# Optimization experiments

Hardware: AMD Instinct MI355X
Metric: run time of the kernel (lower is better)

The kernel has to match this reference:

```python
import jax, jax.numpy as jnp
import numpy as np

C = 64
K = 3  # kernel_size
B, H, W = 8, 128, 128


def conv2d(x, w, b, pad, groups=1):
    y = jax.lax.conv_general_dilated(
        x, w, window_strides=(1, 1), padding=[(pad, pad), (pad, pad)],
        feature_group_count=groups, dimension_numbers=('NCHW', 'OIHW', 'NCHW'))
    return y + b[None, :, None, None]


def setup_inputs() -> dict:
    key = jax.random.key(0)
    ks = jax.random.split(key, 11)
    s3 = 1.0 / np.sqrt(C * 9)  # kaiming-ish scale for 3x3 convs
    inp = {
        'x':  jax.random.normal(ks[0], (B, C, H, W), jnp.float32),
        'w0': jax.random.normal(ks[1], (C, C, 3, 3), jnp.float32) * s3,
        'b0': jax.random.normal(ks[2], (C,), jnp.float32) * 0.01,
        'w1': jax.random.normal(ks[3], (C, 1, 3, 3), jnp.float32) * (1.0 / 3.0),  # depthwise
        'b1': jax.random.normal(ks[4], (C,), jnp.float32) * 0.01,
        'w2': jax.random.normal(ks[5], (1, 1, K), jnp.float32) * (1.0 / np.sqrt(K)),  # conv1d over channel axis
        'b2': jax.random.normal(ks[6], (1,), jnp.float32) * 0.01,
        'w3': jax.random.normal(ks[7], (C * K * K, C, 1, 1), jnp.float32) * (1.0 / np.sqrt(C)),  # 1x1 -> dynamic filters
        'b3': jax.random.normal(ks[8], (C * K * K,), jnp.float32) * 0.01,
        'wf': jax.random.normal(ks[9], (C, C, 3, 3), jnp.float32) * s3,
        'bf': jax.random.normal(ks[10], (C,), jnp.float32) * 0.01,
    }
    return inp


def reference(x, w0, b0, w1, b1, w2, b2, w3, b3, wf, bf):
    b, c, h, w = x.shape
    pre = x
    # conv0: dense 3x3
    x0 = conv2d(x, w0, b0, pad=1)
    # conv1: depthwise 3x3
    x1 = conv2d(x0, w1, b1, pad=1, groups=c)
    # ECA-style channel attention: global avg pool -> conv1d over channel dim
    m = jnp.mean(x0, axis=(2, 3))  # [b, c]
    x2 = jax.lax.conv_general_dilated(
        m[:, None, :], w2, window_strides=(1,), padding=[(K // 2, K // 2)],
        dimension_numbers=('NCH', 'OIH', 'NCH')) + b2[None, :, None]  # [b, 1, c]
    out = x1 + x2[:, 0, :, None, None]  # broadcast [b,c,1,1] over h,w
    # conv3: 1x1 producing per-pixel dynamic filters [b, c*9, h, w]
    fil = jnp.einsum('oc,bchw->bohw', w3[:, :, 0, 0], out) + b3[None, :, None, None]
    filter_x = fil.reshape(b, c, K * K, h, w)
    # unfold(x0): 3x3 patches, channel-major then row-major kernel positions
    xp = jnp.pad(x0, ((0, 0), (0, 0), (1, 1), (1, 1)))
    unfold_x = jnp.stack(
        [xp[:, :, i:i + h, j:j + w] for i in range(3) for j in range(3)], axis=2)  # [b,c,9,h,w]
    out = jnp.sum(unfold_x * filter_x, axis=2)  # per-pixel dynamic conv
    out = jnp.where(out >= 0, out, 0.2 * out)  # LeakyReLU(0.2)
    out = conv2d(out, wf, bf, pad=1) + pre
    return out
```

## Files before the change

kernel.cpp:

```cpp
#include <hip/hip_runtime.h>

#define BB 8
#define C 64
#define HH 128
#define WW 128
#define HW (HH*WW)

#define TS 72
#define NPX 324

typedef __attribute__((ext_vector_type(8))) short short8;
typedef __attribute__((ext_vector_type(4))) float f32x4;

__device__ inline unsigned short f2bf(float f) {
    union { float f; unsigned u; } v; v.f = f;
    unsigned r = v.u + 0x7fff + ((v.u >> 16) & 1);
    return (unsigned short)(r >> 16);
}
__device__ inline float bf2f(unsigned short h) {
    union { unsigned u; float f; } v; v.u = ((unsigned)h) << 16;
    return v.f;
}

__global__ __launch_bounds__(256) void prep_kernel(
    const float* __restrict__ w0, const float* __restrict__ wf,
    const float* __restrict__ w3, const float* __restrict__ b3,
    unsigned short* __restrict__ wb0, unsigned short* __restrict__ wbf,
    unsigned short* __restrict__ wb3, float* __restrict__ b3r,
    float* __restrict__ m)
{
    const int t = blockIdx.x * 256 + threadIdx.x;
    for (int i = t; i < C*C*9; i += 32*256) {
        int p = i % 9; int rest = i / 9; int ci = rest % C; int oc = rest / C;
        wb0[(p*C + oc)*C + ci] = f2bf(w0[i]);
        wbf[(p*C + oc)*C + ci] = f2bf(wf[i]);
    }
    for (int i = t; i < 9*C*C; i += 32*256) {
        int j = i >> 12, oc = (i >> 6) & 63, k = i & 63;
        wb3[i] = f2bf(w3[(oc*9 + j)*C + k]);
    }
    for (int i = t; i < 9*C; i += 32*256) {
        int j = i >> 6, oc = i & 63;
        b3r[i] = b3[oc*9 + j];
    }
    for (int i = t; i < BB*C; i += 32*256) m[i] = 0.f;
}

template<bool FIRST>
__global__ __launch_bounds__(256) void conv_mfma_kernel(
    const void* __restrict__ in,
    const unsigned short* __restrict__ wb,
    const float* __restrict__ bias,
    const float* __restrict__ res,
    void* __restrict__ outp)
{
    __shared__ unsigned short tile[NPX*TS];
    const int b  = blockIdx.z;
    const int h0 = blockIdx.y * 16;
    const int w0 = blockIdx.x * 16;
    const int t  = threadIdx.x;

    {
        const int pxi = t & 31, g = t >> 5;
        for (int px = pxi; px < NPX; px += 32) {
            int th = px / 18, tw = px - th*18;
            int gh = h0 + th - 1, gw = w0 + tw - 1;
            short8 v = {0,0,0,0,0,0,0,0};
            if ((unsigned)gh < HH && (unsigned)gw < WW) {
                if (FIRST) {
                    const float* sp = (const float*)in
                        + ((size_t)(b*C + g*8)*HW + gh*WW + gw);
#pragma unroll
                    for (int k = 0; k < 8; ++k) v[k] = (short)f2bf(sp[k*HW]);
                } else {
                    v = *(const short8*)((const unsigned short*)in
                        + ((size_t)(b*HW) + gh*WW + gw)*C + g*8);
                }
            }
            *(short8*)&tile[px*TS + g*8] = v;
        }
    }
    __syncthreads();

    const int wid = t >> 6, ln = t & 63;
    const int l15 = ln & 15, q = ln >> 4;

    f32x4 acc[4][4];
#pragma unroll
    for (int mg = 0; mg < 4; ++mg)
#pragma unroll
        for (int nt = 0; nt < 4; ++nt) acc[mg][nt] = (f32x4){0.f,0.f,0.f,0.f};

#pragma unroll
    for (int p = 0; p < 9; ++p) {
        const int dh = p / 3, dw = p % 3;
#pragma unroll
        for (int ks = 0; ks < 2; ++ks) {
            short8 bfrag[4];
#pragma unroll
            for (int nt = 0; nt < 4; ++nt)
                bfrag[nt] = *(const short8*)&wb[((size_t)(p*C) + nt*16 + l15)*C + ks*32 + q*8];
            short8 afrag[4];
#pragma unroll
            for (int mg = 0; mg < 4; ++mg) {
                const int r = wid*4 + mg;
                afrag[mg] = *(const short8*)&tile[((r+dh)*18 + l15 + dw)*TS + ks*32 + q*8];
            }
#pragma unroll
            for (int mg = 0; mg < 4; ++mg)
#pragma unroll
                for (int nt = 0; nt < 4; ++nt)
                    acc[mg][nt] = __builtin_amdgcn_mfma_f32_16x16x32_bf16(
                        afrag[mg], bfrag[nt], acc[mg][nt], 0, 0, 0);
        }
    }

    if (FIRST) {
        unsigned short* x0 = (unsigned short*)outp;
#pragma unroll
        for (int mg = 0; mg < 4; ++mg) {
            const int hh = h0 + wid*4 + mg;
#pragma unroll
            for (int nt = 0; nt < 4; ++nt) {
                const int oc = nt*16 + l15;
                const float bv = bias[oc];
#pragma unroll
                for (int reg = 0; reg < 4; ++reg) {
                    const int wwp = w0 + q*4 + reg;
                    x0[((size_t)(b*HW) + hh*WW + wwp)*C + oc] = f2bf(acc[mg][nt][reg] + bv);
                }
            }
        }
    } else {
        float* outg = (float*)outp;
#pragma unroll
        for (int mg = 0; mg < 4; ++mg) {
            const int hh = h0 + wid*4 + mg;
#pragma unroll
            for (int nt = 0; nt < 4; ++nt) {
                const int oc = nt*16 + l15;
                const float bv = bias[oc];
                const size_t base = (size_t)(b*C + oc)*HW + hh*WW + w0 + q*4;
                const float4 rv = *(const float4*)&res[base];
                float4 ov;
                ov.x = acc[mg][nt][0] + bv + rv.x;
                ov.y = acc[mg][nt][1] + bv + rv.y;
                ov.z = acc[mg][nt][2] + bv + rv.z;
                ov.w = acc[mg][nt][3] + bv + rv.w;
                *(float4*)&outg[base] = ov;
            }
        }
    }
}

__global__ __launch_bounds__(256) void mean_kernel(
    const unsigned short* __restrict__ x0, float* __restrict__ m)
{
    const int b = blockIdx.x >> 4, slice = blockIdx.x & 15;
    const int t = threadIdx.x;
    const int pxi = t >> 3, g = t & 7;
    const unsigned short* base = x0 + ((size_t)b*HW + slice*1024)*C + g*8;
    float s[8];
#pragma unroll
    for (int k = 0; k < 8; ++k) s[k] = 0.f;
    for (int it = 0; it < 32; ++it) {
        short8 v = *(const short8*)&base[(size_t)(it*32 + pxi)*C];
#pragma unroll
        for (int k = 0; k < 8; ++k) s[k] += bf2f((unsigned short)v[k]);
    }
    __shared__ float red[32][64];
#pragma unroll
    for (int k = 0; k < 8; ++k) red[pxi][g*8+k] = s[k];
    __syncthreads();
    if (t < 64) {
        float acc = 0.f;
        for (int i = 0; i < 32; ++i) acc += red[i][t];
        atomicAdd(&m[b*C + t], acc * (1.f/(float)HW));
    }
}

__global__ __launch_bounds__(256) void fused_kernel(
    const unsigned short* __restrict__ x0,
    const float* __restrict__ w1, const float* __restrict__ b1,
    const float* __restrict__ w2, const float* __restrict__ b2,
    const unsigned short* __restrict__ wb3,
    const float* __restrict__ b3r,
    const float* __restrict__ m,
    unsigned short* __restrict__ y)
{
    __shared__ unsigned short tile[NPX*TS];
    __shared__ unsigned short alds[256*64];
    const int b  = blockIdx.z;
    const int h0 = blockIdx.y * 16;
    const int w0 = blockIdx.x * 16;
    const int t  = threadIdx.x;

    {
        const int pxi = t & 31, g = t >> 5;
        for (int px = pxi; px < NPX; px += 32) {
            int th = px / 18, tw = px - th*18;
            int gh = h0 + th - 1, gw = w0 + tw - 1;
            short8 v = {0,0,0,0,0,0,0,0};
            if ((unsigned)gh < HH && (unsigned)gw < WW)
                v = *(const short8*)&x0[((size_t)(b*HW) + gh*WW + gw)*C + g*8];
            *(short8*)&tile[px*TS + g*8] = v;
        }
    }
    __syncthreads();

    const int r = t >> 4, cc = t & 15;
    const unsigned short* tbase = tile + (r*18 + cc)*TS;

    float outv[64];
    const float w2a = w2[0], w2b = w2[1], w2c = w2[2], b2v = b2[0];
#pragma unroll
    for (int g = 0; g < 8; ++g) {
        float dw8[8];
#pragma unroll
        for (int k = 0; k < 8; ++k) dw8[k] = 0.f;
#pragma unroll
        for (int j = 0; j < 9; ++j) {
            short8 v = *(const short8*)&tbase[((j/3)*18 + (j%3))*TS + g*8];
#pragma unroll
            for (int k = 0; k < 8; ++k)
                dw8[k] = fmaf(w1[(g*8+k)*9 + j], bf2f((unsigned short)v[k]), dw8[k]);
        }
#pragma unroll
        for (int k = 0; k < 8; ++k) {
            const int c = g*8 + k;
            const float mc = m[b*C + c];
            const float mp = (c > 0)  ? m[b*C + c - 1] : 0.f;
            const float mn = (c < 63) ? m[b*C + c + 1] : 0.f;
            outv[c] = dw8[k] + b1[c] + fmaf(w2a, mp, fmaf(w2b, mc, fmaf(w2c, mn, b2v)));
        }
    }

    {
        const int sw = t & 7;
#pragma unroll
        for (int g = 0; g < 8; ++g) {
            short8 v;
#pragma unroll
            for (int k = 0; k < 8; ++k) v[k] = (short)f2bf(outv[g*8 + k]);
            *(short8*)&alds[t*64 + ((g ^ sw) * 8)] = v;
        }
    }
    __syncthreads();

    const int wid = t >> 6, ln = t & 63;
    const int l15 = ln & 15, q = ln >> 4;

    short8 afrag[4][2];
#pragma unroll
    for (int mg = 0; mg < 4; ++mg) {
        const int px = (wid*4 + mg)*16 + l15;
        const int sw = px & 7;
#pragma unroll
        for (int ks = 0; ks < 2; ++ks)
            afrag[mg][ks] = *(const short8*)&alds[px*64 + (((ks*4 + q) ^ sw) * 8)];
    }

    f32x4 y_acc[4][4];
#pragma unroll
    for (int mg = 0; mg < 4; ++mg)
#pragma unroll
        for (int nt = 0; nt < 4; ++nt) y_acc[mg][nt] = (f32x4){0.f,0.f,0.f,0.f};

#pragma unroll
    for (int j = 0; j < 9; ++j) {
        const int dh = j / 3, dw = j % 3;
#pragma unroll
        for (int ntoc = 0; ntoc < 4; ++ntoc) {
            const int oc = ntoc*16 + l15;
            const float b3v = b3r[j*64 + oc];
            const short8 bf0 = *(const short8*)&wb3[((size_t)(j*64 + oc))*64 + q*8];
            const short8 bf1 = *(const short8*)&wb3[((size_t)(j*64 + oc))*64 + 32 + q*8];
            f32x4 fil[4];
#pragma unroll
            for (int mg = 0; mg < 4; ++mg) {
                f32x4 a = (f32x4){b3v, b3v, b3v, b3v};
                a = __builtin_amdgcn_mfma_f32_16x16x32_bf16(afrag[mg][0], bf0, a, 0, 0, 0);
                a = __builtin_amdgcn_mfma_f32_16x16x32_bf16(afrag[mg][1], bf1, a, 0, 0, 0);
                fil[mg] = a;
            }
#pragma unroll
            for (int mg = 0; mg < 4; ++mg) {
                const int rr = wid*4 + mg;
                const unsigned short* pb = &tile[((rr+dh)*18 + q*4 + dw)*TS + oc];
#pragma unroll
                for (int reg = 0; reg < 4; ++reg) {
                    const float pv = bf2f(pb[reg*TS]);
                    y_acc[mg][ntoc][reg] = fmaf(fil[mg][reg], pv, y_acc[mg][ntoc][reg]);
                }
            }
        }
    }

    __syncthreads();
    unsigned short* ybuf = alds;
#pragma unroll
    for (int mg = 0; mg < 4; ++mg) {
        const int rr = wid*4 + mg;
#pragma unroll
        for (int ntoc = 0; ntoc < 4; ++ntoc) {
            const int oc = ntoc*16 + l15;
#pragma unroll
            for (int reg = 0; reg < 4; ++reg) {
                float v = y_acc[mg][ntoc][reg];
                v = (v >= 0.f) ? v : 0.2f * v;
                ybuf[(rr*16 + q*4 + reg)*64 + oc] = f2bf(v);
            }
        }
    }
    __syncthreads();
    for (int id = t; id < 2048; id += 256) {
        int px = id >> 3, g = id & 7;
        short8 v = *(const short8*)&ybuf[px*64 + g*8];
        int rr = px >> 4, cw = px & 15;
        *(short8*)&y[((size_t)(b*HW) + (h0+rr)*WW + (w0+cw))*C + g*8] = v;
    }
}

extern "C" void kernel_launch(void* const* d_in, const int* in_sizes, int n_in,
                              void* d_out, int out_size, void* d_ws, size_t ws_size,
                              hipStream_t stream) {
    const float* x  = (const float*)d_in[0];
    const float* w0 = (const float*)d_in[1];
    const float* b0 = (const float*)d_in[2];
    const float* w1 = (const float*)d_in[3];
    const float* b1 = (const float*)d_in[4];
    const float* w2 = (const float*)d_in[5];
    const float* b2 = (const float*)d_in[6];
    const float* w3 = (const float*)d_in[7];
    const float* b3 = (const float*)d_in[8];
    const float* wf = (const float*)d_in[9];
    const float* bf = (const float*)d_in[10];
    float* out = (float*)d_out;

    unsigned short* x0  = (unsigned short*)d_ws;
    unsigned short* y   = x0 + (size_t)BB*HW*C;
    float*          m   = (float*)(y + (size_t)BB*HW*C);
    unsigned short* wb0 = (unsigned short*)(m + BB*C);
    unsigned short* wbf = wb0 + 9*C*C;
    unsigned short* wb3 = wbf + 9*C*C;
    float*          b3r = (float*)(wb3 + 9*C*C);

    prep_kernel<<<32, 256, 0, stream>>>(w0, wf, w3, b3, wb0, wbf, wb3, b3r, m);
    conv_mfma_kernel<true><<<dim3(8,8,8), 256, 0, stream>>>(x, wb0, b0, nullptr, x0);
    mean_kernel<<<128, 256, 0, stream>>>(x0, m);
    fused_kernel<<<dim3(8,8,8), 256, 0, stream>>>(x0, w1, b1, w2, b2, wb3, b3r, m, y);
    conv_mfma_kernel<false><<<dim3(8,8,8), 256, 0, stream>>>(y, wbf, bf, x, out);
}
```

Baseline: 223.7 us.

## Fuse channel mean into conv0 epilogue and double threads per block

The channel mean is now computed in the first conv's epilogue with shuffle reductions and atomics, so the separate mean kernel and its re-read of x0 are gone. All three main kernels go from 256 to 512 threads per block, splitting output channels (conv) or rows (fused) across more waves. The fused kernel precomputes the attention bias once per block, uses a transposed depthwise-weight layout for vector loads, swaps MFMA operands so pixel values load as vectors, and swizzles the y staging buffer. In exchange, each wave gets less work, and each conv block now issues 64 extra atomics.

```diff
diff --git a/kernel.cpp b/kernel.cpp
--- a/kernel.cpp
+++ b/kernel.cpp
@@ -10,6 +10,7 @@
 #define NPX 324
 
 typedef __attribute__((ext_vector_type(8))) short short8;
+typedef __attribute__((ext_vector_type(4))) unsigned short us4;
 typedef __attribute__((ext_vector_type(4))) float f32x4;
 
 __device__ inline unsigned short f2bf(float f) {
@@ -25,9 +26,10 @@
 __global__ __launch_bounds__(256) void prep_kernel(
     const float* __restrict__ w0, const float* __restrict__ wf,
     const float* __restrict__ w3, const float* __restrict__ b3,
+    const float* __restrict__ w1,
     unsigned short* __restrict__ wb0, unsigned short* __restrict__ wbf,
     unsigned short* __restrict__ wb3, float* __restrict__ b3r,
-    float* __restrict__ m)
+    float* __restrict__ w1r, float* __restrict__ m)
 {
     const int t = blockIdx.x * 256 + threadIdx.x;
     for (int i = t; i < C*C*9; i += 32*256) {
@@ -40,29 +42,32 @@
         wb3[i] = f2bf(w3[(oc*9 + j)*C + k]);
     }
     for (int i = t; i < 9*C; i += 32*256) {
-        int j = i >> 6, oc = i & 63;
-        b3r[i] = b3[oc*9 + j];
+        int j = i >> 6, c = i & 63;
+        b3r[i] = b3[c*9 + j];
+        w1r[i] = w1[c*9 + j];
     }
     for (int i = t; i < BB*C; i += 32*256) m[i] = 0.f;
 }
 
 template<bool FIRST>
-__global__ __launch_bounds__(256) void conv_mfma_kernel(
+__global__ __launch_bounds__(512, 4) void conv_mfma_kernel(
     const void* __restrict__ in,
     const unsigned short* __restrict__ wb,
     const float* __restrict__ bias,
     const float* __restrict__ res,
-    void* __restrict__ outp)
+    void* __restrict__ outp,
+    float* __restrict__ m)
 {
-    __shared__ unsigned short tile[NPX*TS];
+    __shared__ __align__(16) unsigned short tile[NPX*TS];
+    __shared__ __align__(16) float sred[2][2][4][16];
     const int b  = blockIdx.z;
     const int h0 = blockIdx.y * 16;
     const int w0 = blockIdx.x * 16;
     const int t  = threadIdx.x;
 
     {
-        const int pxi = t & 31, g = t >> 5;
-        for (int px = pxi; px < NPX; px += 32) {
+        const int pxi = t & 63, g = t >> 6;
+        for (int px = pxi; px < NPX; px += 64) {
             int th = px / 18, tw = px - th*18;
             int gh = h0 + th - 1, gw = w0 + tw - 1;
             short8 v = {0,0,0,0,0,0,0,0};
@@ -84,61 +89,73 @@
 
     const int wid = t >> 6, ln = t & 63;
     const int l15 = ln & 15, q = ln >> 4;
-
-    f32x4 acc[4][4];
+    const int ng = wid & 1, wr = wid >> 1;
+
+    f32x4 acc[4][2];
 #pragma unroll
     for (int mg = 0; mg < 4; ++mg)
 #pragma unroll
-        for (int nt = 0; nt < 4; ++nt) acc[mg][nt] = (f32x4){0.f,0.f,0.f,0.f};
+        for (int nt = 0; nt < 2; ++nt) acc[mg][nt] = (f32x4){0.f,0.f,0.f,0.f};
 
 #pragma unroll
     for (int p = 0; p < 9; ++p) {
         const int dh = p / 3, dw = p % 3;
 #pragma unroll
         for (int ks = 0; ks < 2; ++ks) {
-            short8 bfrag[4];
-#pragma unroll
-            for (int nt = 0; nt < 4; ++nt)
-                bfrag[nt] = *(const short8*)&wb[((size_t)(p*C) + nt*16 + l15)*C + ks*32 + q*8];
+            short8 bfrag[2];
+#pragma unroll
+            for (int nt = 0; nt < 2; ++nt)
+                bfrag[nt] = *(const short8*)&wb[((size_t)(p*C) + ng*32 + nt*16 + l15)*C + ks*32 + q*8];
             short8 afrag[4];
 #pragma unroll
-            for (int mg = 0; mg < 4; ++mg) {
-                const int r = wid*4 + mg;
-                afrag[mg] = *(const short8*)&tile[((r+dh)*18 + l15 + dw)*TS + ks*32 + q*8];
-            }
-#pragma unroll
             for (int mg = 0; mg < 4; ++mg)
-#pragma unroll
-                for (int nt = 0; nt < 4; ++nt)
+                afrag[mg] = *(const short8*)&tile[((wr*4 + mg + dh)*18 + l15 + dw)*TS + ks*32 + q*8];
+#pragma unroll
+            for (int mg = 0; mg < 4; ++mg)
+#pragma unroll
+                for (int nt = 0; nt < 2; ++nt)
                     acc[mg][nt] = __builtin_amdgcn_mfma_f32_16x16x32_bf16(
                         afrag[mg], bfrag[nt], acc[mg][nt], 0, 0, 0);
         }
     }
 
     if (FIRST) {
-        unsigned short* x0 = (unsigned short*)outp;
-#pragma unroll
-        for (int mg = 0; mg < 4; ++mg) {
-            const int hh = h0 + wid*4 + mg;
-#pragma unroll
-            for (int nt = 0; nt < 4; ++nt) {
-                const int oc = nt*16 + l15;
-                const float bv = bias[oc];
+        unsigned short* x0o = (unsigned short*)outp;
+#pragma unroll
+        for (int nt = 0; nt < 2; ++nt) {
+            const int oc = ng*32 + nt*16 + l15;
+            const float bv = bias[oc];
+            float s = 0.f;
+#pragma unroll
+            for (int mg = 0; mg < 4; ++mg) {
+                const int hh = h0 + wr*4 + mg;
 #pragma unroll
                 for (int reg = 0; reg < 4; ++reg) {
                     const int wwp = w0 + q*4 + reg;
-                    x0[((size_t)(b*HW) + hh*WW + wwp)*C + oc] = f2bf(acc[mg][nt][reg] + bv);
+                    const unsigned short sv = f2bf(acc[mg][nt][reg] + bv);
+                    x0o[((size_t)(b*HW) + hh*WW + wwp)*C + oc] = sv;
+                    s += bf2f(sv);
                 }
             }
+            s += __shfl_xor(s, 16);
+            s += __shfl_xor(s, 32);
+            if (q == 0) sred[ng][nt][wr][l15] = s;
+        }
+        __syncthreads();
+        if (t < 64) {
+            const int g2 = t >> 5, nt2 = (t >> 4) & 1, l2 = t & 15;
+            float s = sred[g2][nt2][0][l2] + sred[g2][nt2][1][l2]
+                    + sred[g2][nt2][2][l2] + sred[g2][nt2][3][l2];
+            atomicAdd(&m[b*C + t], s * (1.f/(float)HW));
         }
     } else {
         float* outg = (float*)outp;
 #pragma unroll
         for (int mg = 0; mg < 4; ++mg) {
-            const int hh = h0 + wid*4 + mg;
-#pragma unroll
-            for (int nt = 0; nt < 4; ++nt) {
-                const int oc = nt*16 + l15;
+            const int hh = h0 + wr*4 + mg;
+#pragma unroll
+            for (int nt = 0; nt < 2; ++nt) {
+                const int oc = ng*32 + nt*16 + l15;
                 const float bv = bias[oc];
                 const size_t base = (size_t)(b*C + oc)*HW + hh*WW + w0 + q*4;
                 const float4 rv = *(const float4*)&res[base];
@@ -153,51 +170,33 @@
     }
 }
 
-__global__ __launch_bounds__(256) void mean_kernel(
-    const unsigned short* __restrict__ x0, float* __restrict__ m)
-{
-    const int b = blockIdx.x >> 4, slice = blockIdx.x & 15;
-    const int t = threadIdx.x;
-    const int pxi = t >> 3, g = t & 7;
-    const unsigned short* base = x0 + ((size_t)b*HW + slice*1024)*C + g*8;
-    float s[8];
-#pragma unroll
-    for (int k = 0; k < 8; ++k) s[k] = 0.f;
-    for (int it = 0; it < 32; ++it) {
-        short8 v = *(const short8*)&base[(size_t)(it*32 + pxi)*C];
-#pragma unroll
-        for (int k = 0; k < 8; ++k) s[k] += bf2f((unsigned short)v[k]);
-    }
-    __shared__ float red[32][64];
-#pragma unroll
-    for (int k = 0; k < 8; ++k) red[pxi][g*8+k] = s[k];
-    __syncthreads();
-    if (t < 64) {
-        float acc = 0.f;
-        for (int i = 0; i < 32; ++i) acc += red[i][t];
-        atomicAdd(&m[b*C + t], acc * (1.f/(float)HW));
-    }
-}
-
-__global__ __launch_bounds__(256) void fused_kernel(
+__global__ __launch_bounds__(512, 4) void fused_kernel(
     const unsigned short* __restrict__ x0,
-    const float* __restrict__ w1, const float* __restrict__ b1,
+    const float* __restrict__ w1r,
+    const float* __restrict__ b1,
     const float* __restrict__ w2, const float* __restrict__ b2,
     const unsigned short* __restrict__ wb3,
     const float* __restrict__ b3r,
     const float* __restrict__ m,
     unsigned short* __restrict__ y)
 {
-    __shared__ unsigned short tile[NPX*TS];
-    __shared__ unsigned short alds[256*64];
+    __shared__ __align__(16) unsigned short tile[NPX*TS];
+    __shared__ __align__(16) unsigned short alds[256*64];
+    __shared__ __align__(16) float att[64];
     const int b  = blockIdx.z;
     const int h0 = blockIdx.y * 16;
     const int w0 = blockIdx.x * 16;
     const int t  = threadIdx.x;
 
+    if (t < 64) {
+        const float mc = m[b*C + t];
+        const float mp = (t > 0)  ? m[b*C + t - 1] : 0.f;
+        const float mn = (t < 63) ? m[b*C + t + 1] : 0.f;
+        att[t] = b1[t] + fmaf(w2[0], mp, fmaf(w2[1], mc, fmaf(w2[2], mn, b2[0])));
+    }
     {
-        const int pxi = t & 31, g = t >> 5;
-        for (int px = pxi; px < NPX; px += 32) {
+        const int pxi = t & 63, g = t >> 6;
+        for (int px = pxi; px < NPX; px += 64) {
             int th = px / 18, tw = px - th*18;
             int gh = h0 + th - 1, gw = w0 + tw - 1;
             short8 v = {0,0,0,0,0,0,0,0};
@@ -208,41 +207,33 @@
     }
     __syncthreads();
 
-    const int r = t >> 4, cc = t & 15;
-    const unsigned short* tbase = tile + (r*18 + cc)*TS;
-
-    float outv[64];
-    const float w2a = w2[0], w2b = w2[1], w2c = w2[2], b2v = b2[0];
-#pragma unroll
-    for (int g = 0; g < 8; ++g) {
-        float dw8[8];
-#pragma unroll
-        for (int k = 0; k < 8; ++k) dw8[k] = 0.f;
-#pragma unroll
-        for (int j = 0; j < 9; ++j) {
-            short8 v = *(const short8*)&tbase[((j/3)*18 + (j%3))*TS + g*8];
-#pragma unroll
-            for (int k = 0; k < 8; ++k)
-                dw8[k] = fmaf(w1[(g*8+k)*9 + j], bf2f((unsigned short)v[k]), dw8[k]);
-        }
-#pragma unroll
-        for (int k = 0; k < 8; ++k) {
-            const int c = g*8 + k;
-            const float mc = m[b*C + c];
-            const float mp = (c > 0)  ? m[b*C + c - 1] : 0.f;
-            const float mn = (c < 63) ? m[b*C + c + 1] : 0.f;
-            outv[c] = dw8[k] + b1[c] + fmaf(w2a, mp, fmaf(w2b, mc, fmaf(w2c, mn, b2v)));
-        }
-    }
-
     {
-        const int sw = t & 7;
-#pragma unroll
-        for (int g = 0; g < 8; ++g) {
-            short8 v;
-#pragma unroll
-            for (int k = 0; k < 8; ++k) v[k] = (short)f2bf(outv[g*8 + k]);
-            *(short8*)&alds[t*64 + ((g ^ sw) * 8)] = v;
+        const int px1 = t >> 1, chalf = t & 1;
+        const int r1 = px1 >> 4, c1 = px1 & 15;
+        const unsigned short* tbase = tile + (r1*18 + c1)*TS + chalf*32;
+        const int sw1 = px1 & 7;
+#pragma unroll
+        for (int g = 0; g < 4; ++g) {
+            const f32x4 a0 = *(const f32x4*)&att[chalf*32 + g*8];
+            const f32x4 a1 = *(const f32x4*)&att[chalf*32 + g*8 + 4];
+            float dw8[8];
+#pragma unroll
+            for (int k = 0; k < 8; ++k) dw8[k] = (k < 4) ? a0[k] : a1[k-4];
+#pragma unroll
+            for (int j = 0; j < 9; ++j) {
+                short8 v = *(const short8*)&tbase[((j/3)*18 + (j%3))*TS + g*8];
+                const f32x4 wv0 = *(const f32x4*)&w1r[j*64 + chalf*32 + g*8];
+                const f32x4 wv1 = *(const f32x4*)&w1r[j*64 + chalf*32 + g*8 + 4];
+#pragma unroll
+                for (int k = 0; k < 8; ++k)
+                    dw8[k] = fmaf((k < 4) ? wv0[k] : wv1[k-4],
+                                  bf2f((unsigned short)v[k]), dw8[k]);
+            }
+            short8 ov;
+#pragma unroll
+            for (int k = 0; k < 8; ++k) ov[k] = (short)f2bf(dw8[k]);
+            const int kg = chalf*4 + g;
+            *(short8*)&alds[px1*64 + ((kg ^ sw1) * 8)] = ov;
         }
     }
     __syncthreads();
@@ -250,19 +241,19 @@
     const int wid = t >> 6, ln = t & 63;
     const int l15 = ln & 15, q = ln >> 4;
 
-    short8 afrag[4][2];
-#pragma unroll
-    for (int mg = 0; mg < 4; ++mg) {
-        const int px = (wid*4 + mg)*16 + l15;
+    short8 afrag[2][2];
+#pragma unroll
+    for (int mg = 0; mg < 2; ++mg) {
+        const int px = (wid*2 + mg)*16 + l15;
         const int sw = px & 7;
 #pragma unroll
         for (int ks = 0; ks < 2; ++ks)
             afrag[mg][ks] = *(const short8*)&alds[px*64 + (((ks*4 + q) ^ sw) * 8)];
     }
 
-    f32x4 y_acc[4][4];
-#pragma unroll
-    for (int mg = 0; mg < 4; ++mg)
+    f32x4 y_acc[2][4];
+#pragma unroll
+    for (int mg = 0; mg < 2; ++mg)
 #pragma unroll
         for (int nt = 0; nt < 4; ++nt) y_acc[mg][nt] = (f32x4){0.f,0.f,0.f,0.f};
 
@@ -271,27 +262,20 @@
         const int dh = j / 3, dw = j % 3;
 #pragma unroll
         for (int ntoc = 0; ntoc < 4; ++ntoc) {
-            const int oc = ntoc*16 + l15;
-            const float b3v = b3r[j*64 + oc];
-            const short8 bf0 = *(const short8*)&wb3[((size_t)(j*64 + oc))*64 + q*8];
-            const short8 bf1 = *(const short8*)&wb3[((size_t)(j*64 + oc))*64 + 32 + q*8];
-            f32x4 fil[4];
-#pragma unroll
-            for (int mg = 0; mg < 4; ++mg) {
-                f32x4 a = (f32x4){b3v, b3v, b3v, b3v};
-                a = __builtin_amdgcn_mfma_f32_16x16x32_bf16(afrag[mg][0], bf0, a, 0, 0, 0);
-                a = __builtin_amdgcn_mfma_f32_16x16x32_bf16(afrag[mg][1], bf1, a, 0, 0, 0);
-                fil[mg] = a;
-            }
-#pragma unroll
-            for (int mg = 0; mg < 4; ++mg) {
-                const int rr = wid*4 + mg;
-                const unsigned short* pb = &tile[((rr+dh)*18 + q*4 + dw)*TS + oc];
-#pragma unroll
-                for (int reg = 0; reg < 4; ++reg) {
-                    const float pv = bf2f(pb[reg*TS]);
-                    y_acc[mg][ntoc][reg] = fmaf(fil[mg][reg], pv, y_acc[mg][ntoc][reg]);
-                }
+            const short8 bf0 = *(const short8*)&wb3[((size_t)(j*64 + ntoc*16 + l15))*64 + q*8];
+            const short8 bf1 = *(const short8*)&wb3[((size_t)(j*64 + ntoc*16 + l15))*64 + 32 + q*8];
+            const f32x4 b3v4 = *(const f32x4*)&b3r[j*64 + ntoc*16 + q*4];
+#pragma unroll
+            for (int mg = 0; mg < 2; ++mg) {
+                f32x4 a = b3v4;
+                a = __builtin_amdgcn_mfma_f32_16x16x32_bf16(bf0, afrag[mg][0], a, 0, 0, 0);
+                a = __builtin_amdgcn_mfma_f32_16x16x32_bf16(bf1, afrag[mg][1], a, 0, 0, 0);
+                const int rr = wid*2 + mg;
+                const us4 pv = *(const us4*)
+                    &tile[((rr+dh)*18 + l15 + dw)*TS + ntoc*16 + q*4];
+#pragma unroll
+                for (int reg = 0; reg < 4; ++reg)
+                    y_acc[mg][ntoc][reg] = fmaf(a[reg], bf2f(pv[reg]), y_acc[mg][ntoc][reg]);
             }
         }
     }
@@ -299,23 +283,28 @@
     __syncthreads();
     unsigned short* ybuf = alds;
 #pragma unroll
-    for (int mg = 0; mg < 4; ++mg) {
-        const int rr = wid*4 + mg;
+    for (int mg = 0; mg < 2; ++mg) {
+        const int rr = wid*2 + mg;
+        const int px = rr*16 + l15;
+        const int swy = (px & 7) << 1;
 #pragma unroll
         for (int ntoc = 0; ntoc < 4; ++ntoc) {
-            const int oc = ntoc*16 + l15;
+            us4 ov;
 #pragma unroll
             for (int reg = 0; reg < 4; ++reg) {
                 float v = y_acc[mg][ntoc][reg];
                 v = (v >= 0.f) ? v : 0.2f * v;
-                ybuf[(rr*16 + q*4 + reg)*64 + oc] = f2bf(v);
-            }
-        }
-    }
-    __syncthreads();
-    for (int id = t; id < 2048; id += 256) {
+                ov[reg] = f2bf(v);
+            }
+            const int slot = (ntoc*4 + q) ^ swy;
+            *(us4*)&ybuf[px*64 + slot*4] = ov;
+        }
+    }
+    __syncthreads();
+    for (int id = t; id < 2048; id += 512) {
         int px = id >> 3, g = id & 7;
-        short8 v = *(const short8*)&ybuf[px*64 + g*8];
+        const int swy = (px & 7) << 1;
+        short8 v = *(const short8*)&ybuf[px*64 + ((2*g) ^ swy)*4];
         int rr = px >> 4, cw = px & 15;
         *(short8*)&y[((size_t)(b*HW) + (h0+rr)*WW + (w0+cw))*C + g*8] = v;
     }
@@ -344,10 +333,10 @@
     unsigned short* wbf = wb0 + 9*C*C;
     unsigned short* wb3 = wbf + 9*C*C;
     float*          b3r = (float*)(wb3 + 9*C*C);
-
-    prep_kernel<<<32, 256, 0, stream>>>(w0, wf, w3, b3, wb0, wbf, wb3, b3r, m);
-    conv_mfma_kernel<true><<<dim3(8,8,8), 256, 0, stream>>>(x, wb0, b0, nullptr, x0);
-    mean_kernel<<<128, 256, 0, stream>>>(x0, m);
-    fused_kernel<<<dim3(8,8,8), 256, 0, stream>>>(x0, w1, b1, w2, b2, wb3, b3r, m, y);
-    conv_mfma_kernel<false><<<dim3(8,8,8), 256, 0, stream>>>(y, wbf, bf, x, out);
-}
+    float*          w1r = b3r + 9*C;
+
+    prep_kernel<<<32, 256, 0, stream>>>(w0, wf, w3, b3, w1, wb0, wbf, wb3, b3r, w1r, m);
+    conv_mfma_kernel<true><<<dim3(8,8,8), 512, 0, stream>>>(x, wb0, b0, nullptr, x0, m);
+    fused_kernel<<<dim3(8,8,8), 512, 0, stream>>>(x0, w1r, b1, w2, b2, wb3, b3r, m, y);
+    conv_mfma_kernel<false><<<dim3(8,8,8), 512, 0, stream>>>(y, wbf, bf, x, out, nullptr);
+}
```

Result: slower. 352.7 us (+57.7%).

## Fuse channel mean into conv0 epilogue and transpose dynamic-filter MFMA operands

Applied to the files above, without the earlier changes.

Removes the separate mean kernel: conv0's epilogue now reduces per-channel sums of the bf16 outputs with wave shuffles and shared memory, then issues atomics into m. The fused kernel precomputes the ECA attention plus bias once per block into shared memory. It also swaps the MFMA operand order for the dynamic filter so each lane owns a pixel and four consecutive channels, which allows vector bias loads and vectorized patch reads. The LDS output staging now uses an XOR swizzle to cut bank conflicts. In exchange, conv0 gains an extra block barrier plus the reduction work, and the atomic contention pattern changes.

```diff
diff --git a/kernel.cpp b/kernel.cpp
--- a/kernel.cpp
+++ b/kernel.cpp
@@ -10,6 +10,7 @@
 #define NPX 324
 
 typedef __attribute__((ext_vector_type(8))) short short8;
+typedef __attribute__((ext_vector_type(4))) unsigned short us4;
 typedef __attribute__((ext_vector_type(4))) float f32x4;
 
 __device__ inline unsigned short f2bf(float f) {
@@ -52,9 +53,11 @@
     const unsigned short* __restrict__ wb,
     const float* __restrict__ bias,
     const float* __restrict__ res,
-    void* __restrict__ outp)
+    void* __restrict__ outp,
+    float* __restrict__ m)
 {
-    __shared__ unsigned short tile[NPX*TS];
+    __shared__ __align__(16) unsigned short tile[NPX*TS];
+    __shared__ __align__(16) float sred[4][4][16];
     const int b  = blockIdx.z;
     const int h0 = blockIdx.y * 16;
     const int w0 = blockIdx.x * 16;
@@ -116,20 +119,32 @@
     }
 
     if (FIRST) {
-        unsigned short* x0 = (unsigned short*)outp;
-#pragma unroll
-        for (int mg = 0; mg < 4; ++mg) {
-            const int hh = h0 + wid*4 + mg;
-#pragma unroll
-            for (int nt = 0; nt < 4; ++nt) {
-                const int oc = nt*16 + l15;
-                const float bv = bias[oc];
+        unsigned short* x0o = (unsigned short*)outp;
+#pragma unroll
+        for (int nt = 0; nt < 4; ++nt) {
+            const int oc = nt*16 + l15;
+            const float bv = bias[oc];
+            float s = 0.f;
+#pragma unroll
+            for (int mg = 0; mg < 4; ++mg) {
+                const int hh = h0 + wid*4 + mg;
 #pragma unroll
                 for (int reg = 0; reg < 4; ++reg) {
                     const int wwp = w0 + q*4 + reg;
-                    x0[((size_t)(b*HW) + hh*WW + wwp)*C + oc] = f2bf(acc[mg][nt][reg] + bv);
+                    const unsigned short sv = f2bf(acc[mg][nt][reg] + bv);
+                    x0o[((size_t)(b*HW) + hh*WW + wwp)*C + oc] = sv;
+                    s += bf2f(sv);
                 }
             }
+            s += __shfl_xor(s, 16);
+            s += __shfl_xor(s, 32);
+            if (q == 0) sred[wid][nt][l15] = s;
+        }
+        __syncthreads();
+        if (t < 64) {
+            float s = sred[0][t >> 4][t & 15] + sred[1][t >> 4][t & 15]
+                    + sred[2][t >> 4][t & 15] + sred[3][t >> 4][t & 15];
+            atomicAdd(&m[b*C + t], s * (1.f/(float)HW));
         }
     } else {
         float* outg = (float*)outp;
@@ -153,32 +168,6 @@
     }
 }
 
-__global__ __launch_bounds__(256) void mean_kernel(
-    const unsigned short* __restrict__ x0, float* __restrict__ m)
-{
-    const int b = blockIdx.x >> 4, slice = blockIdx.x & 15;
-    const int t = threadIdx.x;
-    const int pxi = t >> 3, g = t & 7;
-    const unsigned short* base = x0 + ((size_t)b*HW + slice*1024)*C + g*8;
-    float s[8];
-#pragma unroll
-    for (int k = 0; k < 8; ++k) s[k] = 0.f;
-    for (int it = 0; it < 32; ++it) {
-        short8 v = *(const short8*)&base[(size_t)(it*32 + pxi)*C];
-#pragma unroll
-        for (int k = 0; k < 8; ++k) s[k] += bf2f((unsigned short)v[k]);
-    }
-    __shared__ float red[32][64];
-#pragma unroll
-    for (int k = 0; k < 8; ++k) red[pxi][g*8+k] = s[k];
-    __syncthreads();
-    if (t < 64) {
-        float acc = 0.f;
-        for (int i = 0; i < 32; ++i) acc += red[i][t];
-        atomicAdd(&m[b*C + t], acc * (1.f/(float)HW));
-    }
-}
-
 __global__ __launch_bounds__(256) void fused_kernel(
     const unsigned short* __restrict__ x0,
     const float* __restrict__ w1, const float* __restrict__ b1,
@@ -188,13 +177,20 @@
     const float* __restrict__ m,
     unsigned short* __restrict__ y)
 {
-    __shared__ unsigned short tile[NPX*TS];
-    __shared__ unsigned short alds[256*64];
+    __shared__ __align__(16) unsigned short tile[NPX*TS];
+    __shared__ __align__(16) unsigned short alds[256*64];
+    __shared__ __align__(16) float att[64];
     const int b  = blockIdx.z;
     const int h0 = blockIdx.y * 16;
     const int w0 = blockIdx.x * 16;
     const int t  = threadIdx.x;
 
+    if (t < 64) {
+        const float mc = m[b*C + t];
+        const float mp = (t > 0)  ? m[b*C + t - 1] : 0.f;
+        const float mn = (t < 63) ? m[b*C + t + 1] : 0.f;
+        att[t] = b1[t] + fmaf(w2[0], mp, fmaf(w2[1], mc, fmaf(w2[2], mn, b2[0])));
+    }
     {
         const int pxi = t & 31, g = t >> 5;
         for (int px = pxi; px < NPX; px += 32) {
@@ -212,7 +208,6 @@
     const unsigned short* tbase = tile + (r*18 + cc)*TS;
 
     float outv[64];
-    const float w2a = w2[0], w2b = w2[1], w2c = w2[2], b2v = b2[0];
 #pragma unroll
     for (int g = 0; g < 8; ++g) {
         float dw8[8];
@@ -228,10 +223,7 @@
 #pragma unroll
         for (int k = 0; k < 8; ++k) {
             const int c = g*8 + k;
-            const float mc = m[b*C + c];
-            const float mp = (c > 0)  ? m[b*C + c - 1] : 0.f;
-            const float mn = (c < 63) ? m[b*C + c + 1] : 0.f;
-            outv[c] = dw8[k] + b1[c] + fmaf(w2a, mp, fmaf(w2b, mc, fmaf(w2c, mn, b2v)));
+            outv[c] = dw8[k] + att[c];
         }
     }
 
@@ -271,27 +263,20 @@
         const int dh = j / 3, dw = j % 3;
 #pragma unroll
         for (int ntoc = 0; ntoc < 4; ++ntoc) {
-            const int oc = ntoc*16 + l15;
-            const float b3v = b3r[j*64 + oc];
-            const short8 bf0 = *(const short8*)&wb3[((size_t)(j*64 + oc))*64 + q*8];
-            const short8 bf1 = *(const short8*)&wb3[((size_t)(j*64 + oc))*64 + 32 + q*8];
-            f32x4 fil[4];
+            const short8 bf0 = *(const short8*)&wb3[((size_t)(j*64 + ntoc*16 + l15))*64 + q*8];
+            const short8 bf1 = *(const short8*)&wb3[((size_t)(j*64 + ntoc*16 + l15))*64 + 32 + q*8];
+            const f32x4 b3v4 = *(const f32x4*)&b3r[j*64 + ntoc*16 + q*4];
 #pragma unroll
             for (int mg = 0; mg < 4; ++mg) {
-                f32x4 a = (f32x4){b3v, b3v, b3v, b3v};
-                a = __builtin_amdgcn_mfma_f32_16x16x32_bf16(afrag[mg][0], bf0, a, 0, 0, 0);
-                a = __builtin_amdgcn_mfma_f32_16x16x32_bf16(afrag[mg][1], bf1, a, 0, 0, 0);
-                fil[mg] = a;
-            }
-#pragma unroll
-            for (int mg = 0; mg < 4; ++mg) {
+                f32x4 a = b3v4;
+                a = __builtin_amdgcn_mfma_f32_16x16x32_bf16(bf0, afrag[mg][0], a, 0, 0, 0);
+                a = __builtin_amdgcn_mfma_f32_16x16x32_bf16(bf1, afrag[mg][1], a, 0, 0, 0);
                 const int rr = wid*4 + mg;
-                const unsigned short* pb = &tile[((rr+dh)*18 + q*4 + dw)*TS + oc];
-#pragma unroll
-                for (int reg = 0; reg < 4; ++reg) {
-                    const float pv = bf2f(pb[reg*TS]);
-                    y_acc[mg][ntoc][reg] = fmaf(fil[mg][reg], pv, y_acc[mg][ntoc][reg]);
-                }
+                const us4 pv = *(const us4*)
+                    &tile[((rr+dh)*18 + l15 + dw)*TS + ntoc*16 + q*4];
+#pragma unroll
+                for (int reg = 0; reg < 4; ++reg)
+                    y_acc[mg][ntoc][reg] = fmaf(a[reg], bf2f(pv[reg]), y_acc[mg][ntoc][reg]);
             }
         }
     }
@@ -301,21 +286,26 @@
 #pragma unroll
     for (int mg = 0; mg < 4; ++mg) {
         const int rr = wid*4 + mg;
+        const int px = rr*16 + l15;
+        const int swy = (px & 7) << 1;
 #pragma unroll
         for (int ntoc = 0; ntoc < 4; ++ntoc) {
-            const int oc = ntoc*16 + l15;
+            us4 ov;
 #pragma unroll
             for (int reg = 0; reg < 4; ++reg) {
                 float v = y_acc[mg][ntoc][reg];
                 v = (v >= 0.f) ? v : 0.2f * v;
-                ybuf[(rr*16 + q*4 + reg)*64 + oc] = f2bf(v);
-            }
+                ov[reg] = f2bf(v);
+            }
+            const int slot = (ntoc*4 + q) ^ swy;
+            *(us4*)&ybuf[px*64 + slot*4] = ov;
         }
     }
     __syncthreads();
     for (int id = t; id < 2048; id += 256) {
         int px = id >> 3, g = id & 7;
-        short8 v = *(const short8*)&ybuf[px*64 + g*8];
+        const int swy = (px & 7) << 1;
+        short8 v = *(const short8*)&ybuf[px*64 + ((2*g) ^ swy)*4];
         int rr = px >> 4, cw = px & 15;
         *(short8*)&y[((size_t)(b*HW) + (h0+rr)*WW + (w0+cw))*C + g*8] = v;
     }
@@ -346,8 +336,7 @@
     float*          b3r = (float*)(wb3 + 9*C*C);
 
     prep_kernel<<<32, 256, 0, stream>>>(w0, wf, w3, b3, wb0, wbf, wb3, b3r, m);
-    conv_mfma_kernel<true><<<dim3(8,8,8), 256, 0, stream>>>(x, wb0, b0, nullptr, x0);
-    mean_kernel<<<128, 256, 0, stream>>>(x0, m);
+    conv_mfma_kernel<true><<<dim3(8,8,8), 256, 0, stream>>>(x, wb0, b0, nullptr, x0, m);
     fused_kernel<<<dim3(8,8,8), 256, 0, stream>>>(x0, w1, b1, w2, b2, wb3, b3r, m, y);
-    conv_mfma_kernel<false><<<dim3(8,8,8), 256, 0, stream>>>(y, wbf, bf, x, out);
-}
+    conv_mfma_kernel<false><<<dim3(8,8,8), 256, 0, stream>>>(y, wbf, bf, x, out, nullptr);
+}
```

Measured after the change: 234.9 us. 5.0% more time.
